# Kernel tuning notes

Hardware: AMD Instinct MI355X
Metric: run time of the kernel (lower is better)

## Reference

```python
import jax, jax.numpy as jnp
import numpy as np

N = 100000
E = 1600000
IN_DIM = 128
HID = 64
HEADS = 4
OUT_DIM = 64
NEG_SLOPE = 0.2


def _xavier(key, shape):
    fan_in, fan_out = shape[0], shape[1]
    limit = float(np.sqrt(6.0 / (fan_in + fan_out)))
    return jax.random.uniform(key, shape, jnp.float32, -limit, limit)


def setup_inputs() -> dict:
    key = jax.random.key(0)
    ks = jax.random.split(key, 8)
    x = jax.random.normal(ks[0], (N, IN_DIM), jnp.float32)
    edge_index = jax.random.randint(ks[1], (2, E), 0, N, dtype=jnp.int32)
    # Layer 0: in=128 -> heads=4, out=64, concat
    W0 = _xavier(ks[2], (IN_DIM, HEADS * HID))
    a0 = _xavier(ks[3], (HEADS, 2 * HID))
    # Layer 1: in=256 -> heads=4, out=64, concat
    W1 = _xavier(ks[4], (HEADS * HID, HEADS * HID))
    a1 = _xavier(ks[5], (HEADS, 2 * HID))
    # Layer 2 (output): in=256 -> heads=1, out=64, no concat
    W2 = _xavier(ks[6], (HEADS * HID, 1 * OUT_DIM))
    a2 = _xavier(ks[7], (1, 2 * OUT_DIM))
    return {"x": x, "edge_index": edge_index,
            "W0": W0, "a0": a0, "W1": W1, "a1": a1, "W2": W2, "a2": a2}


def gat_layer(x, src, dst, W, a, heads, out_dim, concat):
    n = x.shape[0]
    h = (x @ W).reshape(n, heads, out_dim)            # [N, H, D]
    a_s, a_d = a[:, :out_dim], a[:, out_dim:]          # [H, D] each
    alpha_s = jnp.einsum('nhd,hd->nh', h, a_s)         # [N, H]
    alpha_d = jnp.einsum('nhd,hd->nh', h, a_d)         # [N, H]
    e = jax.nn.leaky_relu(alpha_s[src] + alpha_d[dst], NEG_SLOPE)  # [E, H]
    # segment softmax over edges grouped by destination node
    e_max = jax.lax.stop_gradient(jax.ops.segment_max(e, dst, num_segments=n))
    e_max = jnp.where(jnp.isfinite(e_max), e_max, 0.0)
    e_exp = jnp.exp(e - e_max[dst])                    # [E, H]
    denom = jax.ops.segment_sum(e_exp, dst, num_segments=n)  # [N, H]
    att = e_exp / (denom[dst] + 1e-16)                 # [E, H]
    msg = h[src] * att[:, :, None]                     # [E, H, D]
    out = jax.ops.segment_sum(msg, dst, num_segments=n)  # [N, H, D]
    if concat:
        return out.reshape(n, heads * out_dim)
    return out.mean(axis=1)


def reference(x, edge_index, W0, a0, W1, a1, W2, a2):
    src, dst = edge_index[0], edge_index[1]
    # layer 0 + ELU (dropout is identity in eval mode)
    h = gat_layer(x, src, dst, W0, a0, HEADS, HID, True)
    h = jax.nn.elu(h)
    # layer 1 + ELU
    h = gat_layer(h, src, dst, W1, a1, HEADS, HID, True)
    h = jax.nn.elu(h)
    # output layer: single head, no concat, no activation
    out = gat_layer(h, src, dst, W2, a2, 1, OUT_DIM, False)
    return out
```

## Files before the change

kernel.cpp:

```cpp
#include <hip/hip_runtime.h>
#include <math.h>

#define NEG_SLOPE 0.2f
#define SCHUNK 4096

typedef short short8 __attribute__((ext_vector_type(8)));
typedef float float4v __attribute__((ext_vector_type(4)));
typedef int int2v __attribute__((ext_vector_type(2)));
typedef _Float16 h8 __attribute__((ext_vector_type(8)));

__device__ __forceinline__ unsigned short f2bf(float f) {
    unsigned u = __float_as_uint(f);
    unsigned r = (u + 0x7fff + ((u >> 16) & 1)) >> 16;
    return (unsigned short)r;
}
__device__ __forceinline__ float bf2f(unsigned short h) {
    return __uint_as_float(((unsigned)h) << 16);
}
__device__ __forceinline__ unsigned short f2h(float f) {
    _Float16 t = (_Float16)f;
    return *(unsigned short*)&t;
}

__device__ __forceinline__ void gload_lds16(const void* g, void* l) {
    __builtin_amdgcn_global_load_lds(
        (const __attribute__((address_space(1))) unsigned int*)g,
        (__attribute__((address_space(3))) unsigned int*)l, 16, 0, 0);
}


__global__ __launch_bounds__(256) void hist_kernel(const int* __restrict__ dst, int E,
                                                   int NBUCK, int B1, int* __restrict__ H) {
    __shared__ int hist[256];
    int tid = threadIdx.x;
    for (int j = tid; j < NBUCK; j += 256) hist[j] = 0;
    __syncthreads();
    int base = blockIdx.x * SCHUNK;
    int endi = base + SCHUNK; if (endi > E) endi = E;
    for (int i = base + tid; i < endi; i += 256)
        atomicAdd(&hist[dst[i] >> 9], 1);
    __syncthreads();
    for (int j = tid; j < NBUCK; j += 256)
        H[j * B1 + blockIdx.x] = hist[j];
}

__global__ void scan1_kernel(const int* __restrict__ in, int n, int* __restrict__ bsums) {
    __shared__ int sdata[256];
    int tid = threadIdx.x;
    int base = blockIdx.x * 1024 + tid * 4;
    int s = 0;
#pragma unroll
    for (int j = 0; j < 4; ++j) if (base + j < n) s += in[base + j];
    sdata[tid] = s; __syncthreads();
    for (int off = 128; off > 0; off >>= 1) {
        if (tid < off) sdata[tid] += sdata[tid + off];
        __syncthreads();
    }
    if (tid == 0) bsums[blockIdx.x] = sdata[0];
}

__global__ void scan2_kernel(int* bsums, int nb) {
    __shared__ int sd[128];
    int tid = threadIdx.x;
    int v = (tid < nb) ? bsums[tid] : 0;
    sd[tid] = v; __syncthreads();
    for (int off = 1; off < 128; off <<= 1) {
        int t = (tid >= off) ? sd[tid - off] : 0;
        __syncthreads();
        sd[tid] += t;
        __syncthreads();
    }
    if (tid < nb) bsums[tid] = sd[tid] - v;
}

__global__ void scan3g_kernel(const int* __restrict__ in, int n, const int* __restrict__ bsums,
                              int* __restrict__ outs) {
    __shared__ int sdata[256];
    int tid = threadIdx.x;
    int base = blockIdx.x * 1024 + tid * 4;
    int v[4]; int s = 0;
#pragma unroll
    for (int j = 0; j < 4; ++j) { v[j] = (base + j < n) ? in[base + j] : 0; s += v[j]; }
    sdata[tid] = s; __syncthreads();
    for (int off = 1; off < 256; off <<= 1) {
        int t = (tid >= off) ? sdata[tid - off] : 0;
        __syncthreads();
        sdata[tid] += t;
        __syncthreads();
    }
    int excl = sdata[tid] - s;
    int run = bsums[blockIdx.x] + excl;
#pragma unroll
    for (int j = 0; j < 4; ++j) {
        if (base + j < n) { outs[base + j] = run; run += v[j]; }
    }
}

__global__ __launch_bounds__(256) void scatter_kernel(
    const int* __restrict__ dst, const int* __restrict__ src, int E,
    int NBUCK, int B1, const int* __restrict__ Hs, int2v* __restrict__ tmp) {
    __shared__ int curs[256];
    int tid = threadIdx.x;
    for (int j = tid; j < NBUCK; j += 256) curs[j] = Hs[j * B1 + blockIdx.x];
    __syncthreads();
    int base = blockIdx.x * SCHUNK;
    int endi = base + SCHUNK; if (endi > E) endi = E;
    for (int i = base + tid; i < endi; i += 256) {
        int d = dst[i], sv = src[i];
        int p = atomicAdd(&curs[d >> 9], 1);
        int2v pr; pr[0] = d; pr[1] = sv;
        tmp[p] = pr;
    }
}

__global__ __launch_bounds__(256) void bucket_kernel(
    const int2v* __restrict__ tmp, const int* __restrict__ Hs,
    int B1, int NBUCK, int E, int n,
    int* __restrict__ row_ptr, int* __restrict__ sperm) {
    int b = blockIdx.x, tid = threadIdx.x;
    int s = Hs[b * B1];
    int e = (b + 1 < NBUCK) ? Hs[(b + 1) * B1] : E;
    int base = b << 9;
    __shared__ int hist[512];
    __shared__ int scanv[512];
    __shared__ int psum[256];
    hist[tid] = 0; hist[tid + 256] = 0;
    __syncthreads();
    for (int i = s + tid; i < e; i += 256)
        atomicAdd(&hist[tmp[i][0] - base], 1);
    __syncthreads();
    int a = hist[2 * tid], c = hist[2 * tid + 1];
    psum[tid] = a + c;
    __syncthreads();
    for (int off = 1; off < 256; off <<= 1) {
        int t = (tid >= off) ? psum[tid - off] : 0;
        __syncthreads();
        psum[tid] += t;
        __syncthreads();
    }
    int excl = psum[tid] - (a + c);
    scanv[2 * tid] = excl;
    scanv[2 * tid + 1] = excl + a;
    __syncthreads();
    for (int j = tid; j < 512; j += 256) {
        int node = base + j;
        if (node < n) row_ptr[node] = s + scanv[j];
    }
    if (b == 0 && tid == 0) row_ptr[n] = E;
    __syncthreads();
    for (int i = s + tid; i < e; i += 256) {
        int2v pr = tmp[i];
        int p = s + atomicAdd(&scanv[pr[0] - base], 1);
        sperm[p] = pr[1];
    }
}


__global__ __launch_bounds__(256) void prep_kernel(
    const float* __restrict__ W0, const float* __restrict__ W1, const float* __restrict__ W2,
    const float* __restrict__ a0, const float* __restrict__ a1, const float* __restrict__ a2,
    unsigned short* __restrict__ WT0, unsigned short* __restrict__ WT1, unsigned short* __restrict__ WT2,
    unsigned short* __restrict__ wa0, unsigned short* __restrict__ wa1, unsigned short* __restrict__ wa2) {
    int i = blockIdx.x * 256 + threadIdx.x;
    if (i < 32768) {
        int k = i >> 8, n = i & 255;
        WT0[n * 128 + k] = f2bf(W0[i]);
    } else if (i < 98304) {
        int j = i - 32768;
        int k = j >> 8, n = j & 255;
        WT1[n * 256 + k] = f2bf(W1[j]);
    } else if (i < 114688) {
        int j = i - 98304;
        int k = j >> 6, n = j & 63;
        WT2[n * 256 + k] = f2bf(W2[j]);
    } else if (i < 114688 + 2048) {
        int t = i - 114688;
        int k = t >> 4, j8 = t & 15;
        float s = 0.f;
        if (j8 < 8) {
            int h = j8 & 3, off = (j8 >> 2) * 64;
            for (int d = 0; d < 64; ++d)
                s += W0[k * 256 + h * 64 + d] * a0[h * 128 + off + d];
        }
        wa0[j8 * 128 + k] = f2bf(s);
    } else if (i < 114688 + 2048 + 4096) {
        int t = i - 114688 - 2048;
        int k = t >> 4, j8 = t & 15;
        float s = 0.f;
        if (j8 < 8) {
            int h = j8 & 3, off = (j8 >> 2) * 64;
            for (int d = 0; d < 64; ++d)
                s += W1[k * 256 + h * 64 + d] * a1[h * 128 + off + d];
        }
        wa1[j8 * 256 + k] = f2bf(s);
    } else if (i < 114688 + 2048 + 4096 + 4096) {
        int t = i - 114688 - 2048 - 4096;
        int k = t >> 4, j8 = t & 15;
        float s = 0.f;
        if (j8 < 2) {
            for (int d = 0; d < 64; ++d)
                s += W2[k * 64 + d] * a2[j8 * 64 + d];
        }
        wa2[j8 * 256 + k] = f2bf(s);
    }
}

__global__ void xcvt_kernel(const float* __restrict__ X, unsigned short* __restrict__ b, int total) {
    int i = blockIdx.x * 256 + threadIdx.x;
    if (i >= total) return;
    b[i] = f2bf(X[i]);
}


template <int BN>
__global__ __launch_bounds__(256) void gemm_fused(
    const unsigned short* __restrict__ A, const unsigned short* __restrict__ WT,
    const unsigned short* __restrict__ waSDT,
    unsigned short* __restrict__ hf16,
    float* __restrict__ as_, float* __restrict__ ad_,
    int M, int K) {
    __shared__ unsigned short AL[128 * 32];
    __shared__ unsigned short BL[BN * 32];
    __shared__ unsigned short WaL[16 * 32];

    int t = threadIdx.x;
    int w = t >> 6, lane = t & 63;
    int q = lane >> 4, i16 = lane & 15;
    int rowBase = blockIdx.x * 128;
    int colBase = blockIdx.y * BN;

    constexpr int MT = (BN == 128) ? 4 : 2;
    int wrow = (BN == 128) ? (w >> 1) * 64 : w * 32;
    int wcol = (BN == 128) ? (w & 1) * 64 : 0;

    bool alphaBlk = (blockIdx.y == 0);
    bool alphaWave = alphaBlk && ((BN == 64) || ((w & 1) == 0));

    float4v acc[MT][4];
    float4v accA[MT];
#pragma unroll
    for (int mt = 0; mt < MT; ++mt) {
        accA[mt] = (float4v)(0.f);
#pragma unroll
        for (int nt = 0; nt < 4; ++nt) acc[mt][nt] = (float4v)(0.f);
    }

    int srow = t >> 2;
    int skq = (t & 3) * 8;

    for (int k0 = 0; k0 < K; k0 += 32) {
        gload_lds16(A + (size_t)(rowBase + srow) * K + k0 + skq, AL + w * 512);
        gload_lds16(A + (size_t)(rowBase + 64 + srow) * K + k0 + skq, AL + 2048 + w * 512);
        gload_lds16(WT + (size_t)(colBase + srow) * K + k0 + skq, BL + w * 512);
        if (BN == 128)
            gload_lds16(WT + (size_t)(colBase + 64 + srow) * K + k0 + skq, BL + 2048 + w * 512);
        if (alphaBlk && w == 0)
            gload_lds16(waSDT + (size_t)srow * K + k0 + skq, WaL);
        __syncthreads();

        short8 af[MT], bf[4];
#pragma unroll
        for (int mt = 0; mt < MT; ++mt)
            af[mt] = *(short8*)&AL[(wrow + mt * 16 + i16) * 32 + q * 8];
#pragma unroll
        for (int nt = 0; nt < 4; ++nt)
            bf[nt] = *(short8*)&BL[(wcol + nt * 16 + i16) * 32 + q * 8];
#pragma unroll
        for (int mt = 0; mt < MT; ++mt)
#pragma unroll
            for (int nt = 0; nt < 4; ++nt)
                acc[mt][nt] = __builtin_amdgcn_mfma_f32_16x16x32_bf16(af[mt], bf[nt], acc[mt][nt], 0, 0, 0);
        if (alphaWave) {
            short8 aw = *(short8*)&WaL[i16 * 32 + q * 8];
#pragma unroll
            for (int mt = 0; mt < MT; ++mt)
                accA[mt] = __builtin_amdgcn_mfma_f32_16x16x32_bf16(af[mt], aw, accA[mt], 0, 0, 0);
        }
        __syncthreads();
    }

    int cb0 = colBase + wcol;
#pragma unroll
    for (int mt = 0; mt < MT; ++mt)
#pragma unroll
        for (int r = 0; r < 4; ++r) {
            int grow = rowBase + wrow + mt * 16 + q * 4 + r;
            bool ok = grow < M;
            if (ok) {
#pragma unroll
                for (int nt = 0; nt < 4; ++nt) {
                    float v = acc[mt][nt][r];
                    if (BN == 128) hf16[(size_t)grow * 256 + cb0 + nt * 16 + i16] = f2h(v);
                    else           hf16[(size_t)grow * 64 + nt * 16 + i16] = f2h(v);
                }
                if (alphaWave) {
                    float av = accA[mt][r];
                    if (BN == 128) {
                        if (i16 < 4)      as_[grow * 4 + i16] = av;
                        else if (i16 < 8) ad_[grow * 4 + (i16 - 4)] = av;
                    } else {
                        if (i16 == 0)      as_[grow] = av;
                        else if (i16 == 1) ad_[grow] = av;
                    }
                }
            }
        }
}


__global__ __launch_bounds__(256) void aggregate4(
    const unsigned short* __restrict__ hf16, const int* __restrict__ row_ptr,
    const int* __restrict__ sperm, const float* __restrict__ as_, const float* __restrict__ ad_,
    unsigned short* __restrict__ outB, int n) {
    int w = threadIdx.x >> 6, lane = threadIdx.x & 63;
    int node = blockIdx.x * 4 + w;
    if (node >= n) return;
    int beg = row_ptr[node], end = row_ptr[node + 1];
    int deg = end - beg;
    int myh = lane & 3;
    float ad_my = ad_[node * 4 + myh];

    int half = lane >> 5;
    int dg = lane & 31;
    int hh = dg >> 3;
    float acc[8];
#pragma unroll
    for (int k = 0; k < 8; ++k) acc[k] = 0.f;
    float lsum = 0.f;

    const char* hbase = (const char*)hf16;
    unsigned dgo = (unsigned)dg << 4;

    for (int el0 = 0; el0 < deg; el0 += 16) {
        int ne = deg - el0; if (ne > 16) ne = 16;
        int eSlot = lane >> 2;
        float att = 0.f; int sMy = 0;
        if (eSlot < ne) {
            sMy = __builtin_nontemporal_load(&sperm[beg + el0 + eSlot]);
            float e = as_[sMy * 4 + myh] + ad_my;
            e = e > 0.f ? e : NEG_SLOPE * e;
            att = __expf(e);
        }
        lsum += att;

        int j = 0;
        for (; j + 8 <= ne; j += 8) {
            int sl0 = j + half, sl1 = j + 2 + half, sl2 = j + 4 + half, sl3 = j + 6 + half;
            float a0 = __shfl(att, sl0 * 4 + hh, 64);
            int   s0 = __shfl(sMy, sl0 * 4, 64);
            float a1 = __shfl(att, sl1 * 4 + hh, 64);
            int   s1 = __shfl(sMy, sl1 * 4, 64);
            float a2 = __shfl(att, sl2 * 4 + hh, 64);
            int   s2 = __shfl(sMy, sl2 * 4, 64);
            float a3 = __shfl(att, sl3 * 4 + hh, 64);
            int   s3 = __shfl(sMy, sl3 * 4, 64);
            h8 v0 = *(const h8*)(hbase + (((unsigned)s0 << 9) + dgo));
            h8 v1 = *(const h8*)(hbase + (((unsigned)s1 << 9) + dgo));
            h8 v2 = *(const h8*)(hbase + (((unsigned)s2 << 9) + dgo));
            h8 v3 = *(const h8*)(hbase + (((unsigned)s3 << 9) + dgo));
#pragma unroll
            for (int k = 0; k < 8; ++k) acc[k] += a0 * (float)v0[k];
#pragma unroll
            for (int k = 0; k < 8; ++k) acc[k] += a1 * (float)v1[k];
#pragma unroll
            for (int k = 0; k < 8; ++k) acc[k] += a2 * (float)v2[k];
#pragma unroll
            for (int k = 0; k < 8; ++k) acc[k] += a3 * (float)v3[k];
        }
        for (; j < ne; j += 2) {
            int sl = j + half;
            float a = __shfl(att, sl * 4 + hh, 64);
            int   s = __shfl(sMy, sl * 4, 64);
            h8 v = *(const h8*)(hbase + (((unsigned)s << 9) + dgo));
#pragma unroll
            for (int k = 0; k < 8; ++k) acc[k] += a * (float)v[k];
        }
    }

#pragma unroll
    for (int m = 4; m < 64; m <<= 1) lsum += __shfl_xor(lsum, m, 64);
    float inv = 1.f / (lsum + 1e-16f);
    float invh = __shfl(inv, hh, 64);

#pragma unroll
    for (int k = 0; k < 8; ++k) {
        acc[k] += __shfl_xor(acc[k], 32, 64);
        acc[k] *= invh;
    }

    if (half == 0) {
        short8 hv;
#pragma unroll
        for (int k = 0; k < 8; ++k) {
            float o = acc[k] > 0.f ? acc[k] : (__expf(acc[k]) - 1.f);
            hv[k] = (short)f2bf(o);
        }
        __builtin_nontemporal_store(hv, (short8*)(outB + (size_t)node * 256 + dg * 8));
    }
}


__global__ __launch_bounds__(256) void aggregate1(
    const unsigned short* __restrict__ hf16, const int* __restrict__ row_ptr,
    const int* __restrict__ sperm, const float* __restrict__ as_, const float* __restrict__ ad_,
    float* __restrict__ out, int n) {
    int w = threadIdx.x >> 6, lane = threadIdx.x & 63;
    int node = blockIdx.x * 4 + w;
    if (node >= n) return;
    int beg = row_ptr[node], end = row_ptr[node + 1];
    int deg = end - beg;
    float ad_n = ad_[node];

    int eg = lane >> 3;
    int dg = lane & 7;
    float acc[8];
#pragma unroll
    for (int k = 0; k < 8; ++k) acc[k] = 0.f;
    float lsum = 0.f;

    const char* hbase = (const char*)hf16;
    unsigned dgo = (unsigned)dg << 4;

    for (int el0 = 0; el0 < deg; el0 += 64) {
        int ne = deg - el0; if (ne > 64) ne = 64;
        float att = 0.f; int sMy = 0;
        if (lane < ne) {
            sMy = __builtin_nontemporal_load(&sperm[beg + el0 + lane]);
            float e = as_[sMy] + ad_n;
            e = e > 0.f ? e : NEG_SLOPE * e;
            att = __expf(e);
        }
        lsum += att;

        int j = 0;
        for (; j + 32 <= ne; j += 32) {
            int sl0 = j + eg, sl1 = j + 8 + eg, sl2 = j + 16 + eg, sl3 = j + 24 + eg;
            float a0 = __shfl(att, sl0, 64);
            int   s0 = __shfl(sMy, sl0, 64);
            float a1 = __shfl(att, sl1, 64);
            int   s1 = __shfl(sMy, sl1, 64);
            float a2 = __shfl(att, sl2, 64);
            int   s2 = __shfl(sMy, sl2, 64);
            float a3 = __shfl(att, sl3, 64);
            int   s3 = __shfl(sMy, sl3, 64);
            h8 v0 = *(const h8*)(hbase + (((unsigned)s0 << 7) + dgo));
            h8 v1 = *(const h8*)(hbase + (((unsigned)s1 << 7) + dgo));
            h8 v2 = *(const h8*)(hbase + (((unsigned)s2 << 7) + dgo));
            h8 v3 = *(const h8*)(hbase + (((unsigned)s3 << 7) + dgo));
#pragma unroll
            for (int k = 0; k < 8; ++k) acc[k] += a0 * (float)v0[k];
#pragma unroll
            for (int k = 0; k < 8; ++k) acc[k] += a1 * (float)v1[k];
#pragma unroll
            for (int k = 0; k < 8; ++k) acc[k] += a2 * (float)v2[k];
#pragma unroll
            for (int k = 0; k < 8; ++k) acc[k] += a3 * (float)v3[k];
        }
        for (; j < ne; j += 8) {
            int sl = j + eg;
            float a = __shfl(att, sl, 64);
            int   s = __shfl(sMy, sl, 64);
            h8 v = *(const h8*)(hbase + (((unsigned)s << 7) + dgo));
#pragma unroll
            for (int k = 0; k < 8; ++k) acc[k] += a * (float)v[k];
        }
    }

#pragma unroll
    for (int m = 1; m < 64; m <<= 1) lsum += __shfl_xor(lsum, m, 64);
    float inv = 1.f / (lsum + 1e-16f);

#pragma unroll
    for (int m = 8; m < 64; m <<= 1)
#pragma unroll
        for (int k = 0; k < 8; ++k) acc[k] += __shfl_xor(acc[k], m, 64);

    if (eg == 0) {
        float4v o0, o1;
        o0[0] = acc[0] * inv; o0[1] = acc[1] * inv; o0[2] = acc[2] * inv; o0[3] = acc[3] * inv;
        o1[0] = acc[4] * inv; o1[1] = acc[5] * inv; o1[2] = acc[6] * inv; o1[3] = acc[7] * inv;
        __builtin_nontemporal_store(o0, (float4v*)(out + (size_t)node * 64 + dg * 8));
        __builtin_nontemporal_store(o1, (float4v*)(out + (size_t)node * 64 + dg * 8 + 4));
    }
}


extern "C" void kernel_launch(void* const* d_in, const int* in_sizes, int n_in,
                              void* d_out, int out_size, void* d_ws, size_t ws_size,
                              hipStream_t stream) {
    const float* x  = (const float*)d_in[0];
    const int*   ei = (const int*)d_in[1];
    const float* W0 = (const float*)d_in[2];
    const float* a0 = (const float*)d_in[3];
    const float* W1 = (const float*)d_in[4];
    const float* a1 = (const float*)d_in[5];
    const float* W2 = (const float*)d_in[6];
    const float* a2 = (const float*)d_in[7];
    float* out = (float*)d_out;

    int N = in_sizes[0] / 128;
    int E = in_sizes[1] / 2;
    int Npad = (N + 127) & ~127;
    const int* srcp = ei;
    const int* dstp = ei + E;

    char* ws = (char*)d_ws;
    size_t off = 0;
    auto alloc = [&](size_t bytes) -> void* {
        void* p = ws + off;
        off += (bytes + 255) & ~(size_t)255;
        return p;
    };
    unsigned short* xbf  = (unsigned short*)alloc((size_t)Npad * 128 * 2);
    unsigned short* actB = (unsigned short*)alloc((size_t)Npad * 256 * 2);
    unsigned short* hf16 = (unsigned short*)alloc((size_t)Npad * 256 * 2);
    unsigned short* Cf16 = (unsigned short*)alloc((size_t)Npad * 64 * 2);
    float* as_    = (float*)alloc((size_t)N * 4 * 4);
    float* ad_    = (float*)alloc((size_t)N * 4 * 4);
    int*   row_ptr= (int*)alloc((size_t)(N + 1) * 4);
    int*   sperm  = (int*)alloc((size_t)E * 4);
    unsigned short* WT0 = (unsigned short*)alloc((size_t)256 * 128 * 2);
    unsigned short* WT1 = (unsigned short*)alloc((size_t)256 * 256 * 2);
    unsigned short* WT2 = (unsigned short*)alloc((size_t)64 * 256 * 2);
    unsigned short* wa0 = (unsigned short*)alloc((size_t)16 * 128 * 2);
    unsigned short* wa1 = (unsigned short*)alloc((size_t)16 * 256 * 2);
    unsigned short* wa2 = (unsigned short*)alloc((size_t)16 * 256 * 2);
    int*   bsums  = (int*)alloc(4096);

    int B1 = (E + SCHUNK - 1) / SCHUNK;
    int NBUCK = (N + 511) >> 9;
    int Hn = NBUCK * B1;
    int*   H   = (int*)alloc((size_t)Hn * 4);
    int*   Hs  = (int*)alloc((size_t)Hn * 4);
    int2v* tmp = (int2v*)alloc((size_t)E * 8);

    hist_kernel<<<B1, 256, 0, stream>>>(dstp, E, NBUCK, B1, H);
    int nbH = (Hn + 1023) / 1024;
    scan1_kernel<<<nbH, 256, 0, stream>>>(H, Hn, bsums);
    scan2_kernel<<<1, 128, 0, stream>>>(bsums, nbH);
    scan3g_kernel<<<nbH, 256, 0, stream>>>(H, Hn, bsums, Hs);
    scatter_kernel<<<B1, 256, 0, stream>>>(dstp, srcp, E, NBUCK, B1, Hs, tmp);
    bucket_kernel<<<NBUCK, 256, 0, stream>>>(tmp, Hs, B1, NBUCK, E, N, row_ptr, sperm);

    prep_kernel<<<(114688 + 10240 + 255) / 256, 256, 0, stream>>>(
        W0, W1, W2, a0, a1, a2, WT0, WT1, WT2, wa0, wa1, wa2);
    xcvt_kernel<<<((N * 128) + 255) / 256, 256, 0, stream>>>(x, xbf, N * 128);

    int gemm_gx = Npad / 128;
    int ngrid4 = (N + 3) / 4;

    gemm_fused<128><<<dim3(gemm_gx, 2), 256, 0, stream>>>(xbf, WT0, wa0, hf16, as_, ad_, N, 128);
    aggregate4<<<ngrid4, 256, 0, stream>>>(hf16, row_ptr, sperm, as_, ad_, actB, N);

    gemm_fused<128><<<dim3(gemm_gx, 2), 256, 0, stream>>>(actB, WT1, wa1, hf16, as_, ad_, N, 256);
    aggregate4<<<ngrid4, 256, 0, stream>>>(hf16, row_ptr, sperm, as_, ad_, actB, N);

    gemm_fused<64><<<dim3(gemm_gx, 1), 256, 0, stream>>>(actB, WT2, wa2, Cf16, as_, ad_, N, 256);
    aggregate1<<<ngrid4, 256, 0, stream>>>(Cf16, row_ptr, sperm, as_, ad_, out, N);
}
```

Before: 574.9 us.

## Stage gathered neighbor rows into LDS via direct global-to-LDS loads in aggregation

Both aggregation kernels now issue all neighbor-row gathers for an edge chunk as asynchronous global-to-LDS loads into a per-wave slab. The attention exponentials are computed while those loads are in flight, and a single vmcnt wait precedes accumulation from LDS. The goal is more memory-level parallelism and overlap of gather latency with the softmax math. In exchange, each block uses 32KB of LDS, which can lower occupancy, and the explicit waits serialize each chunk's loads against its compute.

```diff
diff --git a/kernel.cpp b/kernel.cpp
--- a/kernel.cpp
+++ b/kernel.cpp
@@ -3,6 +3,9 @@
 
 #define NEG_SLOPE 0.2f
 #define SCHUNK 4096
+
+#define VMCNT0   asm volatile("s_waitcnt vmcnt(0)" ::: "memory")
+#define LGKMCNT0 asm volatile("s_waitcnt lgkmcnt(0)" ::: "memory")
 
 typedef short short8 __attribute__((ext_vector_type(8)));
 typedef float float4v __attribute__((ext_vector_type(4)));
@@ -312,7 +315,9 @@
     const unsigned short* __restrict__ hf16, const int* __restrict__ row_ptr,
     const int* __restrict__ sperm, const float* __restrict__ as_, const float* __restrict__ ad_,
     unsigned short* __restrict__ outB, int n) {
+    __shared__ char slab[4][8192];
     int w = threadIdx.x >> 6, lane = threadIdx.x & 63;
+    char* myslab = slab[w];
     int node = blockIdx.x * 4 + w;
     if (node >= n) return;
     int beg = row_ptr[node], end = row_ptr[node + 1];
@@ -330,50 +335,39 @@
 
     const char* hbase = (const char*)hf16;
     unsigned dgo = (unsigned)dg << 4;
+    unsigned chunk = dgo;
+    int eSlot = lane >> 2;
 
     for (int el0 = 0; el0 < deg; el0 += 16) {
         int ne = deg - el0; if (ne > 16) ne = 16;
-        int eSlot = lane >> 2;
-        float att = 0.f; int sMy = 0;
+        int sMy = 0;
+        if (eSlot < ne) sMy = __builtin_nontemporal_load(&sperm[beg + el0 + eSlot]);
+
+        int nt2 = (ne + 1) >> 1;
+        LGKMCNT0;
+        for (int t = 0; t < nt2; ++t) {
+            int sp = __shfl(sMy, ((2 * t + half) << 2), 64);
+            gload_lds16(hbase + (((size_t)(unsigned)sp) << 9) + chunk, myslab + t * 1024);
+        }
+
+        float att = 0.f;
         if (eSlot < ne) {
-            sMy = __builtin_nontemporal_load(&sperm[beg + el0 + eSlot]);
             float e = as_[sMy * 4 + myh] + ad_my;
             e = e > 0.f ? e : NEG_SLOPE * e;
             att = __expf(e);
         }
         lsum += att;
 
-        int j = 0;
-        for (; j + 8 <= ne; j += 8) {
-            int sl0 = j + half, sl1 = j + 2 + half, sl2 = j + 4 + half, sl3 = j + 6 + half;
-            float a0 = __shfl(att, sl0 * 4 + hh, 64);
-            int   s0 = __shfl(sMy, sl0 * 4, 64);
-            float a1 = __shfl(att, sl1 * 4 + hh, 64);
-            int   s1 = __shfl(sMy, sl1 * 4, 64);
-            float a2 = __shfl(att, sl2 * 4 + hh, 64);
-            int   s2 = __shfl(sMy, sl2 * 4, 64);
-            float a3 = __shfl(att, sl3 * 4 + hh, 64);
-            int   s3 = __shfl(sMy, sl3 * 4, 64);
-            h8 v0 = *(const h8*)(hbase + (((unsigned)s0 << 9) + dgo));
-            h8 v1 = *(const h8*)(hbase + (((unsigned)s1 << 9) + dgo));
-            h8 v2 = *(const h8*)(hbase + (((unsigned)s2 << 9) + dgo));
-            h8 v3 = *(const h8*)(hbase + (((unsigned)s3 << 9) + dgo));
-#pragma unroll
-            for (int k = 0; k < 8; ++k) acc[k] += a0 * (float)v0[k];
-#pragma unroll
-            for (int k = 0; k < 8; ++k) acc[k] += a1 * (float)v1[k];
-#pragma unroll
-            for (int k = 0; k < 8; ++k) acc[k] += a2 * (float)v2[k];
-#pragma unroll
-            for (int k = 0; k < 8; ++k) acc[k] += a3 * (float)v3[k];
-        }
-        for (; j < ne; j += 2) {
-            int sl = j + half;
-            float a = __shfl(att, sl * 4 + hh, 64);
-            int   s = __shfl(sMy, sl * 4, 64);
-            h8 v = *(const h8*)(hbase + (((unsigned)s << 9) + dgo));
-#pragma unroll
-            for (int k = 0; k < 8; ++k) acc[k] += a * (float)v[k];
+        VMCNT0;
+#pragma unroll
+        for (int i = 0; i < 8; ++i) {
+            if (i < nt2) {
+                int j = 2 * i + half;
+                float a = __shfl(att, (j << 2) + hh, 64);
+                h8 v = *(const h8*)(myslab + j * 512 + dgo);
+#pragma unroll
+                for (int k = 0; k < 8; ++k) acc[k] += a * (float)v[k];
+            }
         }
     }
 
@@ -404,7 +398,9 @@
     const unsigned short* __restrict__ hf16, const int* __restrict__ row_ptr,
     const int* __restrict__ sperm, const float* __restrict__ as_, const float* __restrict__ ad_,
     float* __restrict__ out, int n) {
+    __shared__ char slab[4][8192];
     int w = threadIdx.x >> 6, lane = threadIdx.x & 63;
+    char* myslab = slab[w];
     int node = blockIdx.x * 4 + w;
     if (node >= n) return;
     int beg = row_ptr[node], end = row_ptr[node + 1];
@@ -418,51 +414,41 @@
     for (int k = 0; k < 8; ++k) acc[k] = 0.f;
     float lsum = 0.f;
 
-    const char* hbase = (const char*)hf16;
+    const char* cbase = (const char*)hf16;
     unsigned dgo = (unsigned)dg << 4;
+    int rowsel = lane >> 3;
+    unsigned chunk = (unsigned)(lane & 7) << 4;
 
     for (int el0 = 0; el0 < deg; el0 += 64) {
         int ne = deg - el0; if (ne > 64) ne = 64;
-        float att = 0.f; int sMy = 0;
+        int sMy = 0;
+        if (lane < ne) sMy = __builtin_nontemporal_load(&sperm[beg + el0 + lane]);
+
+        int nt8 = (ne + 7) >> 3;
+        LGKMCNT0;
+        for (int t = 0; t < nt8; ++t) {
+            int sp = __shfl(sMy, 8 * t + rowsel, 64);
+            gload_lds16(cbase + (((size_t)(unsigned)sp) << 7) + chunk, myslab + t * 1024);
+        }
+
+        float att = 0.f;
         if (lane < ne) {
-            sMy = __builtin_nontemporal_load(&sperm[beg + el0 + lane]);
             float e = as_[sMy] + ad_n;
             e = e > 0.f ? e : NEG_SLOPE * e;
             att = __expf(e);
         }
         lsum += att;
 
-        int j = 0;
-        for (; j + 32 <= ne; j += 32) {
-            int sl0 = j + eg, sl1 = j + 8 + eg, sl2 = j + 16 + eg, sl3 = j + 24 + eg;
-            float a0 = __shfl(att, sl0, 64);
-            int   s0 = __shfl(sMy, sl0, 64);
-            float a1 = __shfl(att, sl1, 64);
-            int   s1 = __shfl(sMy, sl1, 64);
-            float a2 = __shfl(att, sl2, 64);
-            int   s2 = __shfl(sMy, sl2, 64);
-            float a3 = __shfl(att, sl3, 64);
-            int   s3 = __shfl(sMy, sl3, 64);
-            h8 v0 = *(const h8*)(hbase + (((unsigned)s0 << 7) + dgo));
-            h8 v1 = *(const h8*)(hbase + (((unsigned)s1 << 7) + dgo));
-            h8 v2 = *(const h8*)(hbase + (((unsigned)s2 << 7) + dgo));
-            h8 v3 = *(const h8*)(hbase + (((unsigned)s3 << 7) + dgo));
-#pragma unroll
-            for (int k = 0; k < 8; ++k) acc[k] += a0 * (float)v0[k];
-#pragma unroll
-            for (int k = 0; k < 8; ++k) acc[k] += a1 * (float)v1[k];
-#pragma unroll
-            for (int k = 0; k < 8; ++k) acc[k] += a2 * (float)v2[k];
-#pragma unroll
-            for (int k = 0; k < 8; ++k) acc[k] += a3 * (float)v3[k];
-        }
-        for (; j < ne; j += 8) {
-            int sl = j + eg;
-            float a = __shfl(att, sl, 64);
-            int   s = __shfl(sMy, sl, 64);
-            h8 v = *(const h8*)(hbase + (((unsigned)s << 7) + dgo));
-#pragma unroll
-            for (int k = 0; k < 8; ++k) acc[k] += a * (float)v[k];
+        VMCNT0;
+#pragma unroll
+        for (int i = 0; i < 8; ++i) {
+            if (i < nt8) {
+                int j = 8 * i + eg;
+                float a = __shfl(att, j, 64);
+                h8 v = *(const h8*)(myslab + (j << 7) + dgo);
+#pragma unroll
+                for (int k = 0; k < 8; ++k) acc[k] += a * (float)v[k];
+            }
         }
     }
 
```

Measured after the change: 659.8 us. +14.8%, slower.

## Make aggregation kernels grid-stride and prefetch next node's row bounds and sources

Applied to the files above, without the earlier changes.

Both aggregation kernels now use a grid-stride loop over destination nodes with a quarter as many blocks, so each wave processes about four nodes. While one node is being aggregated, the wave loads the next node's row_ptr bounds and its first chunk of source indices, hiding the dependent index-load latency at the start of each node. The intent is to cut per-node startup latency and block launch overhead. The cost is fewer resident waves to hide gather latency, plus extra live registers.

```diff
diff --git a/kernel.cpp b/kernel.cpp
--- a/kernel.cpp
+++ b/kernel.cpp
@@ -313,89 +313,114 @@
     const int* __restrict__ sperm, const float* __restrict__ as_, const float* __restrict__ ad_,
     unsigned short* __restrict__ outB, int n) {
     int w = threadIdx.x >> 6, lane = threadIdx.x & 63;
-    int node = blockIdx.x * 4 + w;
-    if (node >= n) return;
-    int beg = row_ptr[node], end = row_ptr[node + 1];
-    int deg = end - beg;
+    int node0 = blockIdx.x * 4 + w;
+    if (node0 >= n) return;
+    int stride = gridDim.x * 4;
+
     int myh = lane & 3;
-    float ad_my = ad_[node * 4 + myh];
-
     int half = lane >> 5;
     int dg = lane & 31;
     int hh = dg >> 3;
-    float acc[8];
-#pragma unroll
-    for (int k = 0; k < 8; ++k) acc[k] = 0.f;
-    float lsum = 0.f;
+    int eSlot = lane >> 2;
 
     const char* hbase = (const char*)hf16;
     unsigned dgo = (unsigned)dg << 4;
 
-    for (int el0 = 0; el0 < deg; el0 += 16) {
-        int ne = deg - el0; if (ne > 16) ne = 16;
-        int eSlot = lane >> 2;
-        float att = 0.f; int sMy = 0;
-        if (eSlot < ne) {
-            sMy = __builtin_nontemporal_load(&sperm[beg + el0 + eSlot]);
-            float e = as_[sMy * 4 + myh] + ad_my;
-            e = e > 0.f ? e : NEG_SLOPE * e;
-            att = __expf(e);
-        }
-        lsum += att;
-
-        int j = 0;
-        for (; j + 8 <= ne; j += 8) {
-            int sl0 = j + half, sl1 = j + 2 + half, sl2 = j + 4 + half, sl3 = j + 6 + half;
-            float a0 = __shfl(att, sl0 * 4 + hh, 64);
-            int   s0 = __shfl(sMy, sl0 * 4, 64);
-            float a1 = __shfl(att, sl1 * 4 + hh, 64);
-            int   s1 = __shfl(sMy, sl1 * 4, 64);
-            float a2 = __shfl(att, sl2 * 4 + hh, 64);
-            int   s2 = __shfl(sMy, sl2 * 4, 64);
-            float a3 = __shfl(att, sl3 * 4 + hh, 64);
-            int   s3 = __shfl(sMy, sl3 * 4, 64);
-            h8 v0 = *(const h8*)(hbase + (((unsigned)s0 << 9) + dgo));
-            h8 v1 = *(const h8*)(hbase + (((unsigned)s1 << 9) + dgo));
-            h8 v2 = *(const h8*)(hbase + (((unsigned)s2 << 9) + dgo));
-            h8 v3 = *(const h8*)(hbase + (((unsigned)s3 << 9) + dgo));
-#pragma unroll
-            for (int k = 0; k < 8; ++k) acc[k] += a0 * (float)v0[k];
-#pragma unroll
-            for (int k = 0; k < 8; ++k) acc[k] += a1 * (float)v1[k];
-#pragma unroll
-            for (int k = 0; k < 8; ++k) acc[k] += a2 * (float)v2[k];
-#pragma unroll
-            for (int k = 0; k < 8; ++k) acc[k] += a3 * (float)v3[k];
-        }
-        for (; j < ne; j += 2) {
-            int sl = j + half;
-            float a = __shfl(att, sl * 4 + hh, 64);
-            int   s = __shfl(sMy, sl * 4, 64);
-            h8 v = *(const h8*)(hbase + (((unsigned)s << 9) + dgo));
-#pragma unroll
-            for (int k = 0; k < 8; ++k) acc[k] += a * (float)v[k];
-        }
-    }
-
-#pragma unroll
-    for (int m = 4; m < 64; m <<= 1) lsum += __shfl_xor(lsum, m, 64);
-    float inv = 1.f / (lsum + 1e-16f);
-    float invh = __shfl(inv, hh, 64);
-
-#pragma unroll
-    for (int k = 0; k < 8; ++k) {
-        acc[k] += __shfl_xor(acc[k], 32, 64);
-        acc[k] *= invh;
-    }
-
-    if (half == 0) {
-        short8 hv;
+    int beg = row_ptr[node0], end = row_ptr[node0 + 1];
+    int sFirst = 0;
+    {
+        int d = end - beg; int ne = d > 16 ? 16 : d;
+        if (eSlot < ne) sFirst = __builtin_nontemporal_load(&sperm[beg + eSlot]);
+    }
+
+    for (int node = node0; node < n; node += stride) {
+        int nxt = node + stride;
+        int nbeg = 0, nend = 0;
+        if (nxt < n) {
+            nbeg = __builtin_nontemporal_load(&row_ptr[nxt]);
+            nend = __builtin_nontemporal_load(&row_ptr[nxt + 1]);
+        }
+        int deg = end - beg;
+        float ad_my = ad_[node * 4 + myh];
+        float acc[8];
+#pragma unroll
+        for (int k = 0; k < 8; ++k) acc[k] = 0.f;
+        float lsum = 0.f;
+
+        for (int el0 = 0; el0 < deg; el0 += 16) {
+            int ne = deg - el0; if (ne > 16) ne = 16;
+            float att = 0.f; int sMy = 0;
+            if (el0 == 0) sMy = sFirst;
+            else if (eSlot < ne) sMy = __builtin_nontemporal_load(&sperm[beg + el0 + eSlot]);
+            if (eSlot < ne) {
+                float e = as_[sMy * 4 + myh] + ad_my;
+                e = e > 0.f ? e : NEG_SLOPE * e;
+                att = __expf(e);
+            }
+            lsum += att;
+
+            int j = 0;
+            for (; j + 8 <= ne; j += 8) {
+                int sl0 = j + half, sl1 = j + 2 + half, sl2 = j + 4 + half, sl3 = j + 6 + half;
+                float a0 = __shfl(att, sl0 * 4 + hh, 64);
+                int   s0 = __shfl(sMy, sl0 * 4, 64);
+                float a1 = __shfl(att, sl1 * 4 + hh, 64);
+                int   s1 = __shfl(sMy, sl1 * 4, 64);
+                float a2 = __shfl(att, sl2 * 4 + hh, 64);
+                int   s2 = __shfl(sMy, sl2 * 4, 64);
+                float a3 = __shfl(att, sl3 * 4 + hh, 64);
+                int   s3 = __shfl(sMy, sl3 * 4, 64);
+                h8 v0 = *(const h8*)(hbase + (((unsigned)s0 << 9) + dgo));
+                h8 v1 = *(const h8*)(hbase + (((unsigned)s1 << 9) + dgo));
+                h8 v2 = *(const h8*)(hbase + (((unsigned)s2 << 9) + dgo));
+                h8 v3 = *(const h8*)(hbase + (((unsigned)s3 << 9) + dgo));
+#pragma unroll
+                for (int k = 0; k < 8; ++k) acc[k] += a0 * (float)v0[k];
+#pragma unroll
+                for (int k = 0; k < 8; ++k) acc[k] += a1 * (float)v1[k];
+#pragma unroll
+                for (int k = 0; k < 8; ++k) acc[k] += a2 * (float)v2[k];
+#pragma unroll
+                for (int k = 0; k < 8; ++k) acc[k] += a3 * (float)v3[k];
+            }
+            for (; j < ne; j += 2) {
+                int sl = j + half;
+                float a = __shfl(att, sl * 4 + hh, 64);
+                int   s = __shfl(sMy, sl * 4, 64);
+                h8 v = *(const h8*)(hbase + (((unsigned)s << 9) + dgo));
+#pragma unroll
+                for (int k = 0; k < 8; ++k) acc[k] += a * (float)v[k];
+            }
+        }
+
+        int sNext = 0;
+        if (nxt < n) {
+            int nd = nend - nbeg; int nne = nd > 16 ? 16 : nd;
+            if (eSlot < nne) sNext = __builtin_nontemporal_load(&sperm[nbeg + eSlot]);
+        }
+
+#pragma unroll
+        for (int m = 4; m < 64; m <<= 1) lsum += __shfl_xor(lsum, m, 64);
+        float inv = 1.f / (lsum + 1e-16f);
+        float invh = __shfl(inv, hh, 64);
+
 #pragma unroll
         for (int k = 0; k < 8; ++k) {
-            float o = acc[k] > 0.f ? acc[k] : (__expf(acc[k]) - 1.f);
-            hv[k] = (short)f2bf(o);
-        }
-        __builtin_nontemporal_store(hv, (short8*)(outB + (size_t)node * 256 + dg * 8));
+            acc[k] += __shfl_xor(acc[k], 32, 64);
+            acc[k] *= invh;
+        }
+
+        if (half == 0) {
+            short8 hv;
+#pragma unroll
+            for (int k = 0; k < 8; ++k) {
+                float o = acc[k] > 0.f ? acc[k] : (__expf(acc[k]) - 1.f);
+                hv[k] = (short)f2bf(o);
+            }
+            __builtin_nontemporal_store(hv, (short8*)(outB + (size_t)node * 256 + dg * 8));
+        }
+
+        beg = nbeg; end = nend; sFirst = sNext;
     }
 }
 
@@ -405,82 +430,106 @@
     const int* __restrict__ sperm, const float* __restrict__ as_, const float* __restrict__ ad_,
     float* __restrict__ out, int n) {
     int w = threadIdx.x >> 6, lane = threadIdx.x & 63;
-    int node = blockIdx.x * 4 + w;
-    if (node >= n) return;
-    int beg = row_ptr[node], end = row_ptr[node + 1];
-    int deg = end - beg;
-    float ad_n = ad_[node];
+    int node0 = blockIdx.x * 4 + w;
+    if (node0 >= n) return;
+    int stride = gridDim.x * 4;
 
     int eg = lane >> 3;
     int dg = lane & 7;
-    float acc[8];
-#pragma unroll
-    for (int k = 0; k < 8; ++k) acc[k] = 0.f;
-    float lsum = 0.f;
-
     const char* hbase = (const char*)hf16;
     unsigned dgo = (unsigned)dg << 4;
 
-    for (int el0 = 0; el0 < deg; el0 += 64) {
-        int ne = deg - el0; if (ne > 64) ne = 64;
-        float att = 0.f; int sMy = 0;
-        if (lane < ne) {
-            sMy = __builtin_nontemporal_load(&sperm[beg + el0 + lane]);
-            float e = as_[sMy] + ad_n;
-            e = e > 0.f ? e : NEG_SLOPE * e;
-            att = __expf(e);
-        }
-        lsum += att;
-
-        int j = 0;
-        for (; j + 32 <= ne; j += 32) {
-            int sl0 = j + eg, sl1 = j + 8 + eg, sl2 = j + 16 + eg, sl3 = j + 24 + eg;
-            float a0 = __shfl(att, sl0, 64);
-            int   s0 = __shfl(sMy, sl0, 64);
-            float a1 = __shfl(att, sl1, 64);
-            int   s1 = __shfl(sMy, sl1, 64);
-            float a2 = __shfl(att, sl2, 64);
-            int   s2 = __shfl(sMy, sl2, 64);
-            float a3 = __shfl(att, sl3, 64);
-            int   s3 = __shfl(sMy, sl3, 64);
-            h8 v0 = *(const h8*)(hbase + (((unsigned)s0 << 7) + dgo));
-            h8 v1 = *(const h8*)(hbase + (((unsigned)s1 << 7) + dgo));
-            h8 v2 = *(const h8*)(hbase + (((unsigned)s2 << 7) + dgo));
-            h8 v3 = *(const h8*)(hbase + (((unsigned)s3 << 7) + dgo));
-#pragma unroll
-            for (int k = 0; k < 8; ++k) acc[k] += a0 * (float)v0[k];
-#pragma unroll
-            for (int k = 0; k < 8; ++k) acc[k] += a1 * (float)v1[k];
-#pragma unroll
-            for (int k = 0; k < 8; ++k) acc[k] += a2 * (float)v2[k];
-#pragma unroll
-            for (int k = 0; k < 8; ++k) acc[k] += a3 * (float)v3[k];
-        }
-        for (; j < ne; j += 8) {
-            int sl = j + eg;
-            float a = __shfl(att, sl, 64);
-            int   s = __shfl(sMy, sl, 64);
-            h8 v = *(const h8*)(hbase + (((unsigned)s << 7) + dgo));
-#pragma unroll
-            for (int k = 0; k < 8; ++k) acc[k] += a * (float)v[k];
-        }
-    }
-
-#pragma unroll
-    for (int m = 1; m < 64; m <<= 1) lsum += __shfl_xor(lsum, m, 64);
-    float inv = 1.f / (lsum + 1e-16f);
-
-#pragma unroll
-    for (int m = 8; m < 64; m <<= 1)
-#pragma unroll
-        for (int k = 0; k < 8; ++k) acc[k] += __shfl_xor(acc[k], m, 64);
-
-    if (eg == 0) {
-        float4v o0, o1;
-        o0[0] = acc[0] * inv; o0[1] = acc[1] * inv; o0[2] = acc[2] * inv; o0[3] = acc[3] * inv;
-        o1[0] = acc[4] * inv; o1[1] = acc[5] * inv; o1[2] = acc[6] * inv; o1[3] = acc[7] * inv;
-        __builtin_nontemporal_store(o0, (float4v*)(out + (size_t)node * 64 + dg * 8));
-        __builtin_nontemporal_store(o1, (float4v*)(out + (size_t)node * 64 + dg * 8 + 4));
+    int beg = row_ptr[node0], end = row_ptr[node0 + 1];
+    int sFirst = 0;
+    {
+        int d = end - beg; int ne = d > 64 ? 64 : d;
+        if (lane < ne) sFirst = __builtin_nontemporal_load(&sperm[beg + lane]);
+    }
+
+    for (int node = node0; node < n; node += stride) {
+        int nxt = node + stride;
+        int nbeg = 0, nend = 0;
+        if (nxt < n) {
+            nbeg = __builtin_nontemporal_load(&row_ptr[nxt]);
+            nend = __builtin_nontemporal_load(&row_ptr[nxt + 1]);
+        }
+        int deg = end - beg;
+        float ad_n = ad_[node];
+        float acc[8];
+#pragma unroll
+        for (int k = 0; k < 8; ++k) acc[k] = 0.f;
+        float lsum = 0.f;
+
+        for (int el0 = 0; el0 < deg; el0 += 64) {
+            int ne = deg - el0; if (ne > 64) ne = 64;
+            float att = 0.f; int sMy = 0;
+            if (el0 == 0) sMy = sFirst;
+            else if (lane < ne) sMy = __builtin_nontemporal_load(&sperm[beg + el0 + lane]);
+            if (lane < ne) {
+                float e = as_[sMy] + ad_n;
+                e = e > 0.f ? e : NEG_SLOPE * e;
+                att = __expf(e);
+            }
+            lsum += att;
+
+            int j = 0;
+            for (; j + 32 <= ne; j += 32) {
+                int sl0 = j + eg, sl1 = j + 8 + eg, sl2 = j + 16 + eg, sl3 = j + 24 + eg;
+                float a0 = __shfl(att, sl0, 64);
+                int   s0 = __shfl(sMy, sl0, 64);
+                float a1 = __shfl(att, sl1, 64);
+                int   s1 = __shfl(sMy, sl1, 64);
+                float a2 = __shfl(att, sl2, 64);
+                int   s2 = __shfl(sMy, sl2, 64);
+                float a3 = __shfl(att, sl3, 64);
+                int   s3 = __shfl(sMy, sl3, 64);
+                h8 v0 = *(const h8*)(hbase + (((unsigned)s0 << 7) + dgo));
+                h8 v1 = *(const h8*)(hbase + (((unsigned)s1 << 7) + dgo));
+                h8 v2 = *(const h8*)(hbase + (((unsigned)s2 << 7) + dgo));
+                h8 v3 = *(const h8*)(hbase + (((unsigned)s3 << 7) + dgo));
+#pragma unroll
+                for (int k = 0; k < 8; ++k) acc[k] += a0 * (float)v0[k];
+#pragma unroll
+                for (int k = 0; k < 8; ++k) acc[k] += a1 * (float)v1[k];
+#pragma unroll
+                for (int k = 0; k < 8; ++k) acc[k] += a2 * (float)v2[k];
+#pragma unroll
+                for (int k = 0; k < 8; ++k) acc[k] += a3 * (float)v3[k];
+            }
+            for (; j < ne; j += 8) {
+                int sl = j + eg;
+                float a = __shfl(att, sl, 64);
+                int   s = __shfl(sMy, sl, 64);
+                h8 v = *(const h8*)(hbase + (((unsigned)s << 7) + dgo));
+#pragma unroll
+                for (int k = 0; k < 8; ++k) acc[k] += a * (float)v[k];
+            }
+        }
+
+        int sNext = 0;
+        if (nxt < n) {
+            int nd = nend - nbeg; int nne = nd > 64 ? 64 : nd;
+            if (lane < nne) sNext = __builtin_nontemporal_load(&sperm[nbeg + lane]);
+        }
+
+#pragma unroll
+        for (int m = 1; m < 64; m <<= 1) lsum += __shfl_xor(lsum, m, 64);
+        float inv = 1.f / (lsum + 1e-16f);
+
+#pragma unroll
+        for (int m = 8; m < 64; m <<= 1)
+#pragma unroll
+            for (int k = 0; k < 8; ++k) acc[k] += __shfl_xor(acc[k], m, 64);
+
+        if (eg == 0) {
+            float4v o0, o1;
+            o0[0] = acc[0] * inv; o0[1] = acc[1] * inv; o0[2] = acc[2] * inv; o0[3] = acc[3] * inv;
+            o1[0] = acc[4] * inv; o1[1] = acc[5] * inv; o1[2] = acc[6] * inv; o1[3] = acc[7] * inv;
+            __builtin_nontemporal_store(o0, (float4v*)(out + (size_t)node * 64 + dg * 8));
+            __builtin_nontemporal_store(o1, (float4v*)(out + (size_t)node * 64 + dg * 8 + 4));
+        }
+
+        beg = nbeg; end = nend; sFirst = sNext;
     }
 }
 
@@ -547,14 +596,14 @@
     xcvt_kernel<<<((N * 128) + 255) / 256, 256, 0, stream>>>(x, xbf, N * 128);
 
     int gemm_gx = Npad / 128;
-    int ngrid4 = (N + 3) / 4;
+    int ngrid16 = (N + 15) / 16;
 
     gemm_fused<128><<<dim3(gemm_gx, 2), 256, 0, stream>>>(xbf, WT0, wa0, hf16, as_, ad_, N, 128);
-    aggregate4<<<ngrid4, 256, 0, stream>>>(hf16, row_ptr, sperm, as_, ad_, actB, N);
+    aggregate4<<<ngrid16, 256, 0, stream>>>(hf16, row_ptr, sperm, as_, ad_, actB, N);
 
     gemm_fused<128><<<dim3(gemm_gx, 2), 256, 0, stream>>>(actB, WT1, wa1, hf16, as_, ad_, N, 256);
-    aggregate4<<<ngrid4, 256, 0, stream>>>(hf16, row_ptr, sperm, as_, ad_, actB, N);
+    aggregate4<<<ngrid16, 256, 0, stream>>>(hf16, row_ptr, sperm, as_, ad_, actB, N);
 
     gemm_fused<64><<<dim3(gemm_gx, 1), 256, 0, stream>>>(actB, WT2, wa2, Cf16, as_, ad_, N, 256);
-    aggregate1<<<ngrid4, 256, 0, stream>>>(Cf16, row_ptr, sperm, as_, ad_, out, N);
-}
+    aggregate1<<<ngrid16, 256, 0, stream>>>(Cf16, row_ptr, sperm, as_, ad_, out, N);
+}
```

New measurement: 597.6 us. 3.9% more time.
